# Kernel optimization log

Hardware: AMD Instinct MI355X
Metric: run time of the kernel (lower is better)

Reference implementation:

```python
import jax, jax.numpy as jnp
import numpy as np

N_NODES = 100000
N_EDGES = 1600000
IN_FEATS = 256
HIDDEN = 128
N_CLASSES = 128
NEG_SLOPE = 0.2


def setup_inputs() -> dict:
    key = jax.random.key(0)
    ks = jax.random.split(key, 12)
    inp = {
        "features": jax.random.normal(ks[0], (N_NODES, IN_FEATS), dtype=jnp.float32),
        "src": jax.random.randint(ks[1], (N_EDGES,), 0, N_NODES, dtype=jnp.int32),
        "dst": jax.random.randint(ks[2], (N_EDGES,), 0, N_NODES, dtype=jnp.int32),
        # layer 1 params (Xavier-ish scale)
        "W1": jax.random.normal(ks[3], (HIDDEN, IN_FEATS), dtype=jnp.float32) / np.sqrt(IN_FEATS),
        "al1": jax.random.normal(ks[4], (HIDDEN,), dtype=jnp.float32) / np.sqrt(HIDDEN),
        "ar1": jax.random.normal(ks[5], (HIDDEN,), dtype=jnp.float32) / np.sqrt(HIDDEN),
        "b1": jnp.zeros((HIDDEN,), dtype=jnp.float32),
        # layer 2 params
        "W2": jax.random.normal(ks[6], (N_CLASSES, HIDDEN), dtype=jnp.float32) / np.sqrt(HIDDEN),
        "al2": jax.random.normal(ks[7], (N_CLASSES,), dtype=jnp.float32) / np.sqrt(N_CLASSES),
        "ar2": jax.random.normal(ks[8], (N_CLASSES,), dtype=jnp.float32) / np.sqrt(N_CLASSES),
        "b2": jnp.zeros((N_CLASSES,), dtype=jnp.float32),
    }
    return inp


def _gat_conv(x, W, attn_l, attn_r, bias, src, dst):
    """Single-head DGL GATConv: fc -> edge leaky-relu scores -> segment softmax over dst -> scatter-sum."""
    h = x @ W.T                                   # [N, D]
    el = h @ attn_l                               # [N]
    er = h @ attn_r                               # [N]
    e = jax.nn.leaky_relu(el[src] + er[dst], NEG_SLOPE)   # [E]
    # numerically stable segment softmax over incoming edges of each dst node
    m = jax.ops.segment_max(e, dst, num_segments=N_NODES)          # [N] (-inf for empty)
    ex = jnp.exp(e - m[dst])                                       # [E]
    s = jax.ops.segment_sum(ex, dst, num_segments=N_NODES)         # [N]
    alpha = ex / s[dst]                                            # [E]
    out = jax.ops.segment_sum(h[src] * alpha[:, None], dst, num_segments=N_NODES)
    return out + bias


def reference(features, src, dst, W1, al1, ar1, b1, W2, al2, ar2, b2):
    x = _gat_conv(features, W1, al1, ar1, b1, src, dst)
    x = jax.nn.elu(x)
    return _gat_conv(x, W2, al2, ar2, b2, src, dst)
```

## Files before the change

### kernel.cpp

```cpp
#include <hip/hip_runtime.h>

typedef unsigned short u16;
typedef unsigned int u32;

#define NEG_SLOPE 0.2f
#define BSHIFT 8
#define MAXBUCK 1024

using short8 = __attribute__((ext_vector_type(8))) short;
using float4v = __attribute__((ext_vector_type(4))) float;
using float2v = __attribute__((ext_vector_type(2))) float;

__device__ __forceinline__ float bfu(u16 v) { return __uint_as_float(((u32)v) << 16); }
__device__ __forceinline__ float bflo(u32 u) { return __uint_as_float(u << 16); }
__device__ __forceinline__ float bfhi(u32 u) { return __uint_as_float(u & 0xffff0000u); }
__device__ __forceinline__ u16 f2bf(float f) {
  u32 x = __float_as_uint(f);
  return (u16)((x + 0x7fffu + ((x >> 16) & 1u)) >> 16);
}
__device__ __forceinline__ float loadf(const void* p, int idx, int isbf) {
  return isbf ? bfu(((const u16*)p)[idx]) : ((const float*)p)[idx];
}

__global__ __launch_bounds__(256) void detect_dtype(const u32* __restrict__ w,
                                                    int nwords, int* __restrict__ flag) {
  __shared__ int cnt;
  if (threadIdx.x == 0) cnt = 0;
  __syncthreads();
  int c = 0;
  for (int i = threadIdx.x; i < nwords; i += 256) {
    u32 e = (w[i] >> 7) & 0xFFu;
    c += (e >= 0x60u && e <= 0x90u) ? 1 : 0;
  }
  atomicAdd(&cnt, c);
  __syncthreads();
  if (threadIdx.x == 0) flag[0] = (cnt * 2 > nwords) ? 1 : 0;
}

__global__ __launch_bounds__(256) void scanA(int* __restrict__ a,
                                             int* __restrict__ bsum, int M) {
  __shared__ int sh[256];
  int t = threadIdx.x;
  int idx = blockIdx.x * 256 + t;
  int v = (idx < M) ? a[idx] : 0;
  sh[t] = v;
  __syncthreads();
  for (int off = 1; off < 256; off <<= 1) {
    int y = (t >= off) ? sh[t - off] : 0;
    __syncthreads();
    sh[t] += y;
    __syncthreads();
  }
  if (idx < M) a[idx] = sh[t] - v;
  if (t == 255) bsum[blockIdx.x] = sh[255];
}

__global__ __launch_bounds__(512) void scanBseq(int* __restrict__ a, int MB) {
  __shared__ int sh[512];
  __shared__ int carry;
  int t = threadIdx.x;
  if (t == 0) carry = 0;
  __syncthreads();
  for (int base = 0; base < MB; base += 512) {
    int v = (base + t < MB) ? a[base + t] : 0;
    sh[t] = v;
    __syncthreads();
    for (int off = 1; off < 512; off <<= 1) {
      int y = (t >= off) ? sh[t - off] : 0;
      __syncthreads();
      sh[t] += y;
      __syncthreads();
    }
    int c0 = carry;
    int excl = sh[t] - v + c0;
    int tot = sh[511];
    __syncthreads();
    if (t == 0) carry = c0 + tot;
    if (base + t < MB) a[base + t] = excl;
    __syncthreads();
  }
}

__global__ __launch_bounds__(256) void part_scatter(const int* __restrict__ src,
                                                    const int* __restrict__ dst,
                                                    const int* __restrict__ Gh,
                                                    const int* __restrict__ bsumA,
                                                    int* __restrict__ pd,
                                                    int* __restrict__ ps,
                                                    int E, int PB, int nbuck) {
  __shared__ int cur[MAXBUCK];
  int t = threadIdx.x;
  int blk = blockIdx.x;
  for (int i = t; i < nbuck; i += 256) {
    int j = i * PB + blk;
    cur[i] = Gh[j] + bsumA[j >> 8];
  }
  __syncthreads();
  int pbase = blk * 4096;
#pragma unroll
  for (int j = 0; j < 16; ++j) {
    int e = pbase + j * 256 + t;
    if (e < E) {
      int d = dst[e];
      int s = src[e];
      u32 b = (u32)d >> BSHIFT;
      if (b < (u32)nbuck) {
        int slot = atomicAdd(&cur[b], 1);
        if ((u32)slot < (u32)E) {
          pd[slot] = d;
          ps[slot] = s;
        }
      }
    }
  }
}

__global__ __launch_bounds__(256) void bucket_sort(const int* __restrict__ pd,
                                                   const int* __restrict__ ps,
                                                   const int* __restrict__ Gh,
                                                   const int* __restrict__ bsumA,
                                                   int* __restrict__ indptr,
                                                   int* __restrict__ ssrc,
                                                   int E, int N, int PB, int nbuck) {
  __shared__ int bins[256];
  __shared__ int sh[256];
  __shared__ int cur[256];
  int t = threadIdx.x;
  int b = blockIdx.x;
  int j0 = b * PB;
  int base = Gh[j0] + bsumA[j0 >> 8];
  int nextb = E;
  if (b + 1 < nbuck) {
    int j1 = (b + 1) * PB;
    nextb = Gh[j1] + bsumA[j1 >> 8];
  }
  int sz = nextb - base;

  bins[t] = 0;
  __syncthreads();
  for (int i = t; i < sz; i += 256) atomicAdd(&bins[pd[base + i] & 255], 1);
  __syncthreads();

  int v = bins[t];
  sh[t] = v;
  __syncthreads();
  for (int off = 1; off < 256; off <<= 1) {
    int y = (t >= off) ? sh[t - off] : 0;
    __syncthreads();
    sh[t] += y;
    __syncthreads();
  }
  int excl = sh[t] - v;
  int node = b * 256 + t;
  if (node < N) indptr[node] = base + excl;
  if (b == 0 && t == 0) indptr[N] = E;
  cur[t] = excl;
  __syncthreads();

  for (int i = t; i < sz; i += 256) {
    int d = pd[base + i];
    int slot = atomicAdd(&cur[d & 255], 1);
    u32 gidx = (u32)(base + slot);
    if (gidx < (u32)E) ssrc[gidx] = ps[base + i];
  }
}

__global__ __launch_bounds__(256) void bsw_build(const void* __restrict__ W,
                                                 u16* __restrict__ Bsw, int K,
                                                 const int* __restrict__ dflag) {
  const int isbf = dflag[0];
  int t = blockIdx.x * 256 + threadIdx.x;
  int total = (K / 32) * 8 * 64;
  if (t >= total) return;
  int lane = t & 63;
  int c = (t >> 6) & 7;
  int ktile = t >> 9;
  int n = lane & 15, q = lane >> 4;
  int col = c * 16 + n;
  u16 vals[8];
#pragma unroll
  for (int j = 0; j < 8; ++j) {
    int k = ktile * 32 + q * 8 + j;
    int idx = col * K + k;
    vals[j] = isbf ? ((const u16*)W)[idx] : f2bf(((const float*)W)[idx]);
  }
  *(uint4*)(Bsw + (size_t)t * 8) = *(uint4*)vals;
}

template <int K>
__device__ __forceinline__ void stage_bsw(const u16* __restrict__ Bsw, u16* Bs, int tid) {
  constexpr int PASSES = (K * 256) / 4096;
  int w = tid >> 6, lane = tid & 63;
#pragma unroll
  for (int i = 0; i < PASSES; ++i) {
    int off = i * 4096 + w * 1024;
    __builtin_amdgcn_global_load_lds(
        (const __attribute__((address_space(1))) u32*)((const char*)Bsw + off + lane * 16),
        (__attribute__((address_space(3))) u32*)((char*)Bs + off), 16, 0, 0);
  }
}

template <int K, int ISBF>
__device__ __forceinline__ void gemm_core(const void* __restrict__ Xv,
                                          const u16* Bs,
                                          const int* mclamp, int q, int lane,
                                          float4v acc[2][8]) {
  constexpr int NT = K / 32;
  const uint4* btb = (const uint4*)Bs + lane;
  if (ISBF) {
    const u16* X0 = (const u16*)Xv + (size_t)mclamp[0] * K + q * 8;
    const u16* X1 = (const u16*)Xv + (size_t)mclamp[1] * K + q * 8;
    short8 a0 = *(const short8*)X0;
    short8 a1 = *(const short8*)X1;
#pragma unroll
    for (int t = 0; t < NT; ++t) {
      short8 n0 = a0, n1 = a1;
      if (t + 1 < NT) {
        n0 = *(const short8*)(X0 + (t + 1) * 32);
        n1 = *(const short8*)(X1 + (t + 1) * 32);
      }
      const uint4* bt = btb + (size_t)t * 8 * 64;
#pragma unroll
      for (int c = 0; c < 8; ++c) {
        uint4 bw = bt[c * 64];
        short8 bf = *(short8*)&bw;
        acc[0][c] = __builtin_amdgcn_mfma_f32_16x16x32_bf16(a0, bf, acc[0][c], 0, 0, 0);
        acc[1][c] = __builtin_amdgcn_mfma_f32_16x16x32_bf16(a1, bf, acc[1][c], 0, 0, 0);
      }
      a0 = n0;
      a1 = n1;
    }
  } else {
    const float* X0 = (const float*)Xv + (size_t)mclamp[0] * K + q * 8;
    const float* X1 = (const float*)Xv + (size_t)mclamp[1] * K + q * 8;
    float4 f00 = *(const float4*)X0, f01 = *(const float4*)(X0 + 4);
    float4 f10 = *(const float4*)X1, f11 = *(const float4*)(X1 + 4);
#pragma unroll
    for (int t = 0; t < NT; ++t) {
      float4 g00 = f00, g01 = f01, g10 = f10, g11 = f11;
      if (t + 1 < NT) {
        g00 = *(const float4*)(X0 + (t + 1) * 32);
        g01 = *(const float4*)(X0 + (t + 1) * 32 + 4);
        g10 = *(const float4*)(X1 + (t + 1) * 32);
        g11 = *(const float4*)(X1 + (t + 1) * 32 + 4);
      }
      u16 t0[8] = {f2bf(f00.x), f2bf(f00.y), f2bf(f00.z), f2bf(f00.w),
                   f2bf(f01.x), f2bf(f01.y), f2bf(f01.z), f2bf(f01.w)};
      u16 t1[8] = {f2bf(f10.x), f2bf(f10.y), f2bf(f10.z), f2bf(f10.w),
                   f2bf(f11.x), f2bf(f11.y), f2bf(f11.z), f2bf(f11.w)};
      short8 a0 = *(short8*)t0;
      short8 a1 = *(short8*)t1;
      const uint4* bt = btb + (size_t)t * 8 * 64;
#pragma unroll
      for (int c = 0; c < 8; ++c) {
        uint4 bw = bt[c * 64];
        short8 bf = *(short8*)&bw;
        acc[0][c] = __builtin_amdgcn_mfma_f32_16x16x32_bf16(a0, bf, acc[0][c], 0, 0, 0);
        acc[1][c] = __builtin_amdgcn_mfma_f32_16x16x32_bf16(a1, bf, acc[1][c], 0, 0, 0);
      }
      f00 = g00; f01 = g01; f10 = g10; f11 = g11;
    }
  }
}

template <int K, int DYNA>
__device__ __forceinline__ void gemm_body(int bix, const void* __restrict__ Xv,
                                          const u16* __restrict__ Bsw,
                                          u16* __restrict__ Hb,
                                          const void* __restrict__ al,
                                          const void* __restrict__ ar,
                                          float* __restrict__ el_,
                                          float* __restrict__ er_, int N,
                                          const int* __restrict__ dflag) {
  __shared__ __align__(16) u16 Bs[(K / 32) * 8 * 64 * 8];
  const int isbfP = dflag[0];
  int tid = threadIdx.x;
  int w = tid >> 6, lane = tid & 63;
  int n = lane & 15, q = lane >> 4;
  int base = bix * 128 + w * 32;

  stage_bsw<K>(Bsw, Bs, tid);

  int mclamp[2];
#pragma unroll
  for (int mt = 0; mt < 2; ++mt) {
    int m = base + mt * 16 + n;
    mclamp[mt] = (m < N) ? m : 0;
  }

  float alv[8], arv[8];
#pragma unroll
  for (int c = 0; c < 8; ++c) {
    alv[c] = loadf(al, c * 16 + n, isbfP);
    arv[c] = loadf(ar, c * 16 + n, isbfP);
  }

  float4v acc[2][8];
#pragma unroll
  for (int mt = 0; mt < 2; ++mt)
#pragma unroll
    for (int c = 0; c < 8; ++c) acc[mt][c] = (float4v){0.f, 0.f, 0.f, 0.f};

  __syncthreads();

  if (DYNA == 0 || isbfP) {
    gemm_core<K, 1>(Xv, Bs, mclamp, q, lane, acc);
  } else {
    gemm_core<K, 0>(Xv, Bs, mclamp, q, lane, acc);
  }

#pragma unroll
  for (int mt = 0; mt < 2; ++mt)
#pragma unroll
    for (int c = 0; c < 8; ++c) {
#pragma unroll
      for (int r = 0; r < 4; ++r) {
        int row = base + mt * 16 + q * 4 + r;
        if (row < N) Hb[(size_t)row * 128 + c * 16 + n] = f2bf(acc[mt][c][r]);
      }
    }

#pragma unroll
  for (int mt = 0; mt < 2; ++mt)
#pragma unroll
    for (int r = 0; r < 4; ++r) {
      float sl = 0.f, sr = 0.f;
#pragma unroll
      for (int c = 0; c < 8; ++c) {
        float v = acc[mt][c][r];
        sl = fmaf(v, alv[c], sl);
        sr = fmaf(v, arv[c], sr);
      }
#pragma unroll
      for (int off = 1; off < 16; off <<= 1) {
        sl += __shfl_xor(sl, off);
        sr += __shfl_xor(sr, off);
      }
      if (n == 0) {
        int row = base + mt * 16 + q * 4 + r;
        if (row < N) {
          el_[row] = sl;
          er_[row] = sr;
        }
      }
    }
}

template <int K, int DYNA>
__global__ __launch_bounds__(256) void gemm_mfma(const void* __restrict__ Xv,
                                                 const u16* __restrict__ Bsw,
                                                 u16* __restrict__ Hb,
                                                 const void* __restrict__ al,
                                                 const void* __restrict__ ar,
                                                 float* __restrict__ el_,
                                                 float* __restrict__ er_, int N,
                                                 const int* __restrict__ dflag) {
  gemm_body<K, DYNA>(blockIdx.x, Xv, Bsw, Hb, al, ar, el_, er_, N, dflag);
}

template <int K, int DYNA>
__global__ __launch_bounds__(256) void fused_gemm_hist(
    const void* __restrict__ Xv, const u16* __restrict__ Bsw, u16* __restrict__ Hb,
    const void* __restrict__ al, const void* __restrict__ ar,
    float* __restrict__ el_, float* __restrict__ er_, int N,
    const int* __restrict__ dflag, int gemm_blocks,
    const int* __restrict__ dst, int* __restrict__ Gh, int E, int PB, int nbuck) {
  __shared__ int hcnt[MAXBUCK];
  int bix = (int)blockIdx.x;
  if (bix < gemm_blocks) {
    gemm_body<K, DYNA>(bix, Xv, Bsw, Hb, al, ar, el_, er_, N, dflag);
    return;
  }
  int pblk = bix - gemm_blocks;
  int t = threadIdx.x;
  for (int i = t; i < nbuck; i += 256) hcnt[i] = 0;
  __syncthreads();
  int pbase = pblk * 4096;
#pragma unroll
  for (int j = 0; j < 16; ++j) {
    int e = pbase + j * 256 + t;
    if (e < E) {
      u32 b = (u32)dst[e] >> BSHIFT;
      if (b < (u32)nbuck) atomicAdd(&hcnt[b], 1);
    }
  }
  __syncthreads();
  for (int i = t; i < nbuck; i += 256) Gh[(size_t)i * PB + pblk] = hcnt[i];
}

template <int MODE>
__global__ __launch_bounds__(256) void agg_kernel(const u32* __restrict__ Hb,
                                                  const float* __restrict__ el,
                                                  const float* __restrict__ er,
                                                  const int* __restrict__ indptr,
                                                  const int* __restrict__ ssrc,
                                                  const void* __restrict__ bias,
                                                  void* __restrict__ outv, int N,
                                                  const int* __restrict__ dflag) {
  const int isbf = dflag[0];
  int tid = threadIdx.x;
  int n = blockIdx.x * 4 + (tid >> 6);
  int lane = tid & 63;
  if (n >= N) return;

  int beg = indptr[n];
  int end = indptr[n + 1];
  int deg = end - beg;
  float ern = er[n];

  float2v acc = {0.f, 0.f};
  float inv;

  if (deg <= 64) {
    int valid = lane < deg;
    int ide = valid ? ssrc[beg + lane] : 0;
    float sc = el[ide] + ern;
    sc = (sc > 0.f) ? sc : NEG_SLOPE * sc;
    sc = valid ? sc : -INFINITY;

    float m = sc;
#pragma unroll
    for (int off = 1; off < 64; off <<= 1) m = fmaxf(m, __shfl_xor(m, off));
    float pe = __expf(sc - m);
    float l = pe;
#pragma unroll
    for (int off = 1; off < 64; off <<= 1) l += __shfl_xor(l, off);

    int e = 0;
    for (; e + 8 <= deg; e += 8) {
      int id_[8];
      u32 h_[8];
#pragma unroll
      for (int k = 0; k < 8; ++k) id_[k] = __builtin_amdgcn_readlane(ide, e + k);
#pragma unroll
      for (int k = 0; k < 8; ++k) h_[k] = Hb[(size_t)id_[k] * 64 + lane];
#pragma unroll
      for (int k = 0; k < 8; ++k) {
        float pk = __int_as_float(__builtin_amdgcn_readlane(__float_as_int(pe), e + k));
        float2v hv = {bflo(h_[k]), bfhi(h_[k])};
        float2v pv = {pk, pk};
        acc = pv * hv + acc;
      }
    }
    for (; e + 4 <= deg; e += 4) {
      int id_[4];
      u32 h_[4];
#pragma unroll
      for (int k = 0; k < 4; ++k) id_[k] = __builtin_amdgcn_readlane(ide, e + k);
#pragma unroll
      for (int k = 0; k < 4; ++k) h_[k] = Hb[(size_t)id_[k] * 64 + lane];
#pragma unroll
      for (int k = 0; k < 4; ++k) {
        float pk = __int_as_float(__builtin_amdgcn_readlane(__float_as_int(pe), e + k));
        float2v hv = {bflo(h_[k]), bfhi(h_[k])};
        float2v pv = {pk, pk};
        acc = pv * hv + acc;
      }
    }
    for (; e < deg; ++e) {
      int i0 = __builtin_amdgcn_readlane(ide, e);
      u32 h0 = Hb[(size_t)i0 * 64 + lane];
      float pk = __int_as_float(__builtin_amdgcn_readlane(__float_as_int(pe), e));
      float2v hv = {bflo(h0), bfhi(h0)};
      float2v pv = {pk, pk};
      acc = pv * hv + acc;
    }
    inv = (deg > 0 && l > 0.f) ? 1.f / l : 0.f;
  } else {
    float m_run = -INFINITY, l_run = 0.f;
    for (int p = beg; p < end; p += 64) {
      int rem = end - p;
      int valid = lane < rem;
      int ide = valid ? ssrc[p + lane] : 0;
      float sc = el[ide] + ern;
      sc = (sc > 0.f) ? sc : NEG_SLOPE * sc;
      sc = valid ? sc : -INFINITY;
      float mc = sc;
#pragma unroll
      for (int off = 1; off < 64; off <<= 1) mc = fmaxf(mc, __shfl_xor(mc, off));
      float m_new = fmaxf(m_run, mc);
      float corr = __expf(m_run - m_new);
      float pe = __expf(sc - m_new);
      float ls = pe;
#pragma unroll
      for (int off = 1; off < 64; off <<= 1) ls += __shfl_xor(ls, off);
      l_run = l_run * corr + ls;
      float2v cv = {corr, corr};
      acc = acc * cv;
      m_run = m_new;

      int cl = (rem < 64) ? rem : 64;
      int e = 0;
      for (; e + 8 <= cl; e += 8) {
        int id_[8];
        u32 h_[8];
#pragma unroll
        for (int k = 0; k < 8; ++k) id_[k] = __builtin_amdgcn_readlane(ide, e + k);
#pragma unroll
        for (int k = 0; k < 8; ++k) h_[k] = Hb[(size_t)id_[k] * 64 + lane];
#pragma unroll
        for (int k = 0; k < 8; ++k) {
          float pk = __int_as_float(__builtin_amdgcn_readlane(__float_as_int(pe), e + k));
          float2v hv = {bflo(h_[k]), bfhi(h_[k])};
          float2v pv = {pk, pk};
          acc = pv * hv + acc;
        }
      }
      for (; e < cl; ++e) {
        int i0 = __builtin_amdgcn_readlane(ide, e);
        u32 h0 = Hb[(size_t)i0 * 64 + lane];
        float pk = __int_as_float(__builtin_amdgcn_readlane(__float_as_int(pe), e));
        float2v hv = {bflo(h0), bfhi(h0)};
        float2v pv = {pk, pk};
        acc = pv * hv + acc;
      }
    }
    inv = (l_run > 0.f) ? 1.f / l_run : 0.f;
  }

  float o0 = acc.x * inv + loadf(bias, 2 * lane, isbf);
  float o1 = acc.y * inv + loadf(bias, 2 * lane + 1, isbf);

  if (MODE == 0) {
    o0 = (o0 > 0.f) ? o0 : (__expf(o0) - 1.f);
    o1 = (o1 > 0.f) ? o1 : (__expf(o1) - 1.f);
    ((u32*)outv)[(size_t)n * 64 + lane] = (u32)f2bf(o0) | ((u32)f2bf(o1) << 16);
  } else {
    if (isbf) {
      ((u32*)outv)[(size_t)n * 64 + lane] = (u32)f2bf(o0) | ((u32)f2bf(o1) << 16);
    } else {
      ((float2*)outv)[(size_t)n * 64 + lane] = make_float2(o0, o1);
    }
  }
}


extern "C" void kernel_launch(void* const* d_in, const int* in_sizes, int n_in,
                              void* d_out, int out_size, void* d_ws, size_t ws_size,
                              hipStream_t stream) {
  const int IN_FEATS = 256, HID = 128;
  const void* features = d_in[0];
  const int* src = (const int*)d_in[1];
  const int* dst = (const int*)d_in[2];
  const void* W1 = d_in[3];
  const void* al1 = d_in[4];
  const void* ar1 = d_in[5];
  const void* b1 = d_in[6];
  const void* W2 = d_in[7];
  const void* al2 = d_in[8];
  const void* ar2 = d_in[9];
  const void* b2 = d_in[10];

  const int N = in_sizes[0] / IN_FEATS;
  const int E = in_sizes[1];

  char* p = (char*)d_ws;
  auto alloc = [&](size_t bytes) -> void* {
    void* q = (void*)p;
    p += (bytes + 255) & ~(size_t)255;
    return q;
  };
  int* dflag = (int*)alloc(256);
  u16* Bsw1 = (u16*)alloc((size_t)(IN_FEATS / 32) * 8 * 64 * 8 * 2);
  u16* Bsw2 = (u16*)alloc((size_t)(HID / 32) * 8 * 64 * 8 * 2);
  u16* hb = (u16*)alloc((size_t)N * HID * 2);
  u16* x = (u16*)alloc((size_t)N * HID * 2);
  float* el = (float*)alloc((size_t)N * 4);
  float* er = (float*)alloc((size_t)N * 4);
  int* indptr = (int*)alloc((size_t)(N + 1) * 4);

  const int nbuck = (N + 255) >> BSHIFT;
  const int PB = (E + 4095) / 4096;
  const int M = nbuck * PB;
  const int MB1 = (M + 255) / 256;

  int* Gh = (int*)alloc((size_t)M * 4);
  int* bsumA = (int*)alloc((size_t)MB1 * 4);
  int* ssrc = (int*)alloc((size_t)E * 4);

  int* pd = (int*)x;
  int* ps = (int*)((char*)x + (((size_t)E * 4 + 255) & ~(size_t)255));

  const int GEMM_B = (N + 127) / 128;
  const int NODE_B = (N + 3) / 4;

  detect_dtype<<<1, 256, 0, stream>>>((const u32*)features, 4096, dflag);
  bsw_build<<<((IN_FEATS / 32) * 8 * 64 + 255) / 256, 256, 0, stream>>>(W1, Bsw1, IN_FEATS, dflag);
  bsw_build<<<((HID / 32) * 8 * 64 + 255) / 256, 256, 0, stream>>>(W2, Bsw2, HID, dflag);

  fused_gemm_hist<IN_FEATS, 1><<<GEMM_B + PB, 256, 0, stream>>>(
      features, Bsw1, hb, al1, ar1, el, er, N, dflag, GEMM_B, dst, Gh, E, PB, nbuck);

  scanA<<<MB1, 256, 0, stream>>>(Gh, bsumA, M);
  scanBseq<<<1, 512, 0, stream>>>(bsumA, MB1);

  part_scatter<<<PB, 256, 0, stream>>>(src, dst, Gh, bsumA, pd, ps, E, PB, nbuck);
  bucket_sort<<<nbuck, 256, 0, stream>>>(pd, ps, Gh, bsumA, indptr, ssrc, E, N, PB, nbuck);

  agg_kernel<0><<<NODE_B, 256, 0, stream>>>((const u32*)hb, el, er, indptr, ssrc, b1, (void*)x, N, dflag);

  gemm_mfma<HID, 0><<<GEMM_B, 256, 0, stream>>>((const void*)x, Bsw2, hb, al2, ar2, el, er, N, dflag);
  agg_kernel<1><<<NODE_B, 256, 0, stream>>>((const u32*)hb, el, er, indptr, ssrc, b2, d_out, N, dflag);
}
```

Before: 452.9 us.

## Read swizzled weights directly from global memory and preload all A tiles

Drops the LDS staging of the pre-swizzled weight matrix and its block barrier, so MFMA B operands are read straight from global memory (and the L2 cache) per wave. The bf16 path now issues every row-tile load up front into a register array instead of double-buffering one tile ahead. This removes the LDS footprint and the sync, which may raise occupancy, but each wave now repeats the weight loads from global memory and register pressure grows with K.

```diff
diff --git a/kernel.cpp b/kernel.cpp
--- a/kernel.cpp
+++ b/kernel.cpp
@@ -187,48 +187,31 @@
   *(uint4*)(Bsw + (size_t)t * 8) = *(uint4*)vals;
 }
 
-template <int K>
-__device__ __forceinline__ void stage_bsw(const u16* __restrict__ Bsw, u16* Bs, int tid) {
-  constexpr int PASSES = (K * 256) / 4096;
-  int w = tid >> 6, lane = tid & 63;
-#pragma unroll
-  for (int i = 0; i < PASSES; ++i) {
-    int off = i * 4096 + w * 1024;
-    __builtin_amdgcn_global_load_lds(
-        (const __attribute__((address_space(1))) u32*)((const char*)Bsw + off + lane * 16),
-        (__attribute__((address_space(3))) u32*)((char*)Bs + off), 16, 0, 0);
-  }
-}
-
 template <int K, int ISBF>
 __device__ __forceinline__ void gemm_core(const void* __restrict__ Xv,
-                                          const u16* Bs,
+                                          const u16* __restrict__ Bsw,
                                           const int* mclamp, int q, int lane,
                                           float4v acc[2][8]) {
   constexpr int NT = K / 32;
-  const uint4* btb = (const uint4*)Bs + lane;
+  const uint4* btb = (const uint4*)Bsw + lane;
   if (ISBF) {
     const u16* X0 = (const u16*)Xv + (size_t)mclamp[0] * K + q * 8;
     const u16* X1 = (const u16*)Xv + (size_t)mclamp[1] * K + q * 8;
-    short8 a0 = *(const short8*)X0;
-    short8 a1 = *(const short8*)X1;
+    short8 a0[NT], a1[NT];
+#pragma unroll
+    for (int t = 0; t < NT; ++t) a0[t] = *(const short8*)(X0 + t * 32);
+#pragma unroll
+    for (int t = 0; t < NT; ++t) a1[t] = *(const short8*)(X1 + t * 32);
 #pragma unroll
     for (int t = 0; t < NT; ++t) {
-      short8 n0 = a0, n1 = a1;
-      if (t + 1 < NT) {
-        n0 = *(const short8*)(X0 + (t + 1) * 32);
-        n1 = *(const short8*)(X1 + (t + 1) * 32);
-      }
       const uint4* bt = btb + (size_t)t * 8 * 64;
 #pragma unroll
       for (int c = 0; c < 8; ++c) {
         uint4 bw = bt[c * 64];
         short8 bf = *(short8*)&bw;
-        acc[0][c] = __builtin_amdgcn_mfma_f32_16x16x32_bf16(a0, bf, acc[0][c], 0, 0, 0);
-        acc[1][c] = __builtin_amdgcn_mfma_f32_16x16x32_bf16(a1, bf, acc[1][c], 0, 0, 0);
-      }
-      a0 = n0;
-      a1 = n1;
+        acc[0][c] = __builtin_amdgcn_mfma_f32_16x16x32_bf16(a0[t], bf, acc[0][c], 0, 0, 0);
+        acc[1][c] = __builtin_amdgcn_mfma_f32_16x16x32_bf16(a1[t], bf, acc[1][c], 0, 0, 0);
+      }
     }
   } else {
     const float* X0 = (const float*)Xv + (size_t)mclamp[0] * K + q * 8;
@@ -272,15 +255,12 @@
                                           float* __restrict__ el_,
                                           float* __restrict__ er_, int N,
                                           const int* __restrict__ dflag) {
-  __shared__ __align__(16) u16 Bs[(K / 32) * 8 * 64 * 8];
   const int isbfP = dflag[0];
   int tid = threadIdx.x;
   int w = tid >> 6, lane = tid & 63;
   int n = lane & 15, q = lane >> 4;
   int base = bix * 128 + w * 32;
 
-  stage_bsw<K>(Bsw, Bs, tid);
-
   int mclamp[2];
 #pragma unroll
   for (int mt = 0; mt < 2; ++mt) {
@@ -301,12 +281,10 @@
 #pragma unroll
     for (int c = 0; c < 8; ++c) acc[mt][c] = (float4v){0.f, 0.f, 0.f, 0.f};
 
-  __syncthreads();
-
   if (DYNA == 0 || isbfP) {
-    gemm_core<K, 1>(Xv, Bs, mclamp, q, lane, acc);
+    gemm_core<K, 1>(Xv, Bsw, mclamp, q, lane, acc);
   } else {
-    gemm_core<K, 0>(Xv, Bs, mclamp, q, lane, acc);
+    gemm_core<K, 0>(Xv, Bsw, mclamp, q, lane, acc);
   }
 
 #pragma unroll
```

After: 463.8 us. 2.4% more time.
